# Kernel tuning notes

Measured on AMD Instinct MI355X. Metric: run time of the kernel, lower is better.

Reference implementation:

```python
import jax, jax.numpy as jnp
import numpy as np

K = 2048          # codes per class
NC = 8            # num_classes
CD = 256          # conv_dims
SP = 4            # latent spatial (28 -> 14 -> 7 -> 4)
D = CD * SP * SP  # 4096 codebook vector dim
N = 512           # RoIs


def _conv(x, W, b, stride, pad):
    y = jax.lax.conv_general_dilated(x, W, (stride, stride), [(pad, pad), (pad, pad)],
                                     dimension_numbers=('NCHW', 'OIHW', 'NCHW'))
    return y + b[None, :, None, None]


def _upsample2_ac(x):
    # bilinear upsample x2 with align_corners=True (torch nn.Upsample semantics)
    n, ch, H, W = x.shape
    Ho, Wo = 2 * H, 2 * W
    ys = jnp.arange(Ho) * (H - 1) / (Ho - 1)
    xs = jnp.arange(Wo) * (W - 1) / (Wo - 1)
    y0 = jnp.floor(ys).astype(jnp.int32); y1 = jnp.minimum(y0 + 1, H - 1)
    x0 = jnp.floor(xs).astype(jnp.int32); x1 = jnp.minimum(x0 + 1, W - 1)
    wy = (ys - y0).astype(x.dtype); wx = (xs - x0).astype(x.dtype)
    r = x[:, :, y0, :] * (1 - wy)[None, None, :, None] + x[:, :, y1, :] * wy[None, None, :, None]
    return r[:, :, :, x0] * (1 - wx)[None, None, None, :] + r[:, :, :, x1] * wx[None, None, None, :]


def setup_inputs() -> dict:
    key = jax.random.key(0)
    ks = jax.random.split(key, 20)
    s = 0.02
    inp = {
        'x': jax.random.normal(ks[0], (N, 1, 28, 28), jnp.float32),
        'We0': jax.random.normal(ks[1], (CD, 1, 3, 3), jnp.float32) * s,
        'be0': jnp.zeros((CD,), jnp.float32),
        'We1': jax.random.normal(ks[2], (CD, CD, 3, 3), jnp.float32) * s,
        'be1': jnp.zeros((CD,), jnp.float32),
        'We2': jax.random.normal(ks[3], (CD, CD, 3, 3), jnp.float32) * s,
        'be2': jnp.zeros((CD,), jnp.float32),
        'E': jax.random.normal(ks[4], (K * NC, D), jnp.float32) * s,
        'Wd0': jax.random.normal(ks[5], (CD, CD, 3, 3), jnp.float32) * s,
        'bd0': jnp.zeros((CD,), jnp.float32),
        'Wd1': jax.random.normal(ks[6], (CD, CD, 3, 3), jnp.float32) * s,
        'bd1': jnp.zeros((CD,), jnp.float32),
        'Wd2': jax.random.normal(ks[7], (CD, CD, 3, 3), jnp.float32) * s,
        'bd2': jnp.zeros((CD,), jnp.float32),
        'Wo': jax.random.normal(ks[8], (1, CD, 3, 3), jnp.float32) * s,
        'bo': jnp.zeros((1,), jnp.float32),
        'c': jax.random.randint(ks[9], (N,), 0, NC, jnp.int32),
    }
    return inp


def reference(x, We0, be0, We1, be1, We2, be2, E, Wd0, bd0, Wd1, bd1, Wd2, bd2, Wo, bo, c):
    # ---- encoder: 3 stride-2 convs, relu on all but the last ----
    h = jax.nn.relu(_conv(x, We0, be0, 2, 1))   # [N,CD,14,14]
    h = jax.nn.relu(_conv(h, We1, be1, 2, 1))   # [N,CD,7,7]
    h = _conv(h, We2, be2, 2, 1)                # [N,CD,4,4]
    z_e = h.reshape(N, D)                       # flattened latent, == z_e_x [N,D,1,1]

    # ---- class-conditional VQ ----
    # torch code loops over unique classes and concatenates -> output is in
    # stable-sorted-by-class order; replicate via stable argsort permutation.
    perm = jnp.argsort(c)  # stable
    # distances to the FULL table, then mask codes outside the sample's class slice
    d2 = (jnp.sum(z_e * z_e, axis=1, keepdims=True)         # [N,1]
          - 2.0 * z_e @ E.T                                  # [N,K*NC]
          + jnp.sum(E * E, axis=1)[None, :])
    code_cls = jnp.arange(K * NC, dtype=c.dtype) // K        # class of each code row
    d2 = jnp.where(code_cls[None, :] == c[:, None], d2, jnp.inf)
    idx = jnp.argmin(d2, axis=1)                             # global code index (includes key*K offset)

    q_det = jax.lax.stop_gradient(E)[idx]                    # vq_st uses detached codebook
    z_q_st = z_e + jax.lax.stop_gradient(q_det - z_e)        # straight-through
    z_q_bar = E[idx]                                         # gradient flows to codebook

    z_q_st_p = z_q_st[perm]
    z_q_bar_p = z_q_bar[perm]

    # ---- decoder: (upsample2 bilinear ac + conv + relu) x3, pad=0 on layer k==num_conv-2 ----
    xd = z_q_st_p.reshape(N, CD, SP, SP)
    xd = jax.nn.relu(_conv(_upsample2_ac(xd), Wd0, bd0, 1, 1))  # 4->8
    xd = jax.nn.relu(_conv(_upsample2_ac(xd), Wd1, bd1, 1, 0))  # 8->16->14
    xd = jax.nn.relu(_conv(_upsample2_ac(xd), Wd2, bd2, 1, 1))  # 14->28
    x_tilde = jax.nn.sigmoid(_conv(xd, Wo, bo, 1, 1))           # [N,1,28,28]

    return (x_tilde, z_e.reshape(N, D, 1, 1), z_q_bar_p.reshape(N, D, 1, 1))
```

## Files before the change

### kernel.cpp

```cpp
#include <hip/hip_runtime.h>
#include <hip/hip_bf16.h>
#include <cstdint>
#include <cstddef>

#define CDIV(a,b) (((a)+(b)-1)/(b))

typedef __attribute__((ext_vector_type(8))) short vbf8;
typedef __attribute__((ext_vector_type(4))) float vf4;

__device__ inline unsigned short f2bf(float f) {
  unsigned u = __float_as_uint(f);
  unsigned r = (u + 0x7fffu + ((u >> 16) & 1u)) >> 16;
  return (unsigned short)r;
}
__device__ inline float bf2f(unsigned short h) { return __uint_as_float(((unsigned)h) << 16); }

__global__ __launch_bounds__(256) void conv_e0_cl_kernel(
    const float* __restrict__ x, const float* __restrict__ W,
    const float* __restrict__ b, unsigned short* __restrict__ hi,
    unsigned short* __restrict__ lo)
{
  __shared__ float s_img[784];
  const int n = blockIdx.x;
  const int co = threadIdx.x;
  for (int i = threadIdx.x; i < 784; i += 256) s_img[i] = x[(size_t)n*784 + i];
  float w[9];
#pragma unroll
  for (int t = 0; t < 9; ++t) w[t] = W[co*9 + t];
  const float bb = b[co];
  __syncthreads();
  for (int p = 0; p < 196; ++p) {
    int y = p / 14, xo = p % 14;
    float a = bb;
#pragma unroll
    for (int t = 0; t < 9; ++t) {
      int yi = 2*y + t/3 - 1, xi = 2*xo + t%3 - 1;
      if (yi >= 0 && yi < 28 && xi >= 0 && xi < 28) a = fmaf(w[t], s_img[yi*28 + xi], a);
    }
    a = fmaxf(a, 0.f);
    unsigned short h = f2bf(a);
    size_t oidx = ((size_t)n*196 + p)*256 + co;
    hi[oidx] = h;
    lo[oidx] = f2bf(a - bf2f(h));
  }
}

__global__ __launch_bounds__(256) void wprep2_kernel(
    const float* __restrict__ W, unsigned short* __restrict__ Whi,
    unsigned short* __restrict__ Wlo)
{
  int idx = blockIdx.x*256 + threadIdx.x;
  if (idx >= 589824) return;
  int j   = idx & 7;
  int co  = (idx >> 3) & 255;
  int cig = (idx >> 11) & 31;
  int t   = idx >> 16;
  int ci  = cig*8 + j;
  float w = W[((size_t)co*256 + ci)*9 + t];
  unsigned short h = f2bf(w);
  Whi[idx] = h;
  Wlo[idx] = f2bf(w - bf2f(h));
}

template<int NFM, int WS>
__device__ __forceinline__ void mfma_block(
    const vbf8* __restrict__ sbuf, const vbf8* __restrict__ wsrc, int cc,
    const int (&abase)[NFM], vf4 (&acc)[NFM][4], int cobase, int l15, int lq)
{
#pragma unroll
  for (int t = 0; t < 9; ++t) {
    const int dy = t/3, dx = t%3;
#pragma unroll
    for (int kk = 0; kk < 2; ++kk) {
      vbf8 bfr[4];
      const int cig_g = cc*8 + kk*4 + lq;
#pragma unroll
      for (int nf = 0; nf < 4; ++nf)
        bfr[nf] = wsrc[((size_t)t*32 + cig_g)*256 + cobase + nf*16 + l15];
      vbf8 af[NFM];
      const int cigl = kk*4 + lq;
#pragma unroll
      for (int mf = 0; mf < NFM; ++mf) {
        int lin = abase[mf] + dy*WS + dx;
        af[mf] = sbuf[(lin*8 + cigl) ^ (lin & 7)];
      }
#pragma unroll
      for (int mf = 0; mf < NFM; ++mf)
#pragma unroll
        for (int nf = 0; nf < 4; ++nf)
          acc[mf][nf] = __builtin_amdgcn_mfma_f32_16x16x32_bf16(af[mf], bfr[nf], acc[mf][nf], 0, 0, 0);
    }
  }
}

template<int STRIDE, int HO, int WO, int X0, int WOP, int ROWS, int HI, int WI,
         int PAD, int ACT, int SPLIT, int OUTMODE, int DBUF>
__global__ __launch_bounds__(256, 2) void convmfma_kernel(
    const unsigned short* __restrict__ inT, const unsigned short* __restrict__ inTlo,
    const vbf8* __restrict__ Wt, const vbf8* __restrict__ Wtlo,
    const float* __restrict__ bias,
    unsigned short* __restrict__ outT, unsigned short* __restrict__ outTlo,
    float* __restrict__ outF)
{
  constexpr int NFM = ROWS*WOP/16;
  constexpr int RIN = (ROWS-1)*STRIDE + 3;
  constexpr int WS  = (WOP-1)*STRIDE + 3;
  constexpr int NG  = SPLIT ? 12 : 4;
  constexpr int NELEM = RIN*WS*8;
  constexpr int CEIL = (NELEM + 255) / 256;
  __shared__ vbf8 sA[DBUF ? 2 : 1][NELEM];

  const int n  = blockIdx.x;
  const int y0 = blockIdx.y * ROWS;
  const int tid = threadIdx.x;
  const int lane = tid & 63;
  const int wv = tid >> 6;
  const int l15 = lane & 15;
  const int lq  = lane >> 4;
  const int cobase = wv * 64;

  int abase[NFM];
#pragma unroll
  for (int mf = 0; mf < NFM; ++mf) {
    int pos = mf*16 + l15;
    abase[mf] = (pos / WOP) * STRIDE * WS + (pos % WOP) * STRIDE;
  }

  vf4 acc[NFM][4];
#pragma unroll
  for (int mf = 0; mf < NFM; ++mf)
#pragma unroll
    for (int nf = 0; nf < 4; ++nf) acc[mf][nf] = (vf4){0.f, 0.f, 0.f, 0.f};

  if constexpr (DBUF) {
    int goff[CEIL];
#pragma unroll
    for (int q = 0; q < CEIL; ++q) {
      int idx = tid + q*256;
      int lin = idx >> 3, cig = idx & 7;
      int rr = lin / WS, xx = lin % WS;
      int yi = y0*STRIDE + rr - PAD, xi = X0*STRIDE + xx - PAD;
      bool ok = (idx < NELEM) && yi >= 0 && yi < HI && xi >= 0 && xi < WI;
      goff[q] = ok ? (int)((((size_t)n*HI + yi)*WI + xi)*256 + cig*8) : -1;
    }
    vbf8 r[CEIL];
#pragma unroll
    for (int q = 0; q < CEIL; ++q) {
      vbf8 v = {0,0,0,0,0,0,0,0};
      if (goff[q] >= 0) v = *(const vbf8*)(inT + goff[q]);
      r[q] = v;
    }
#pragma unroll
    for (int q = 0; q < CEIL; ++q) {
      int idx = tid + q*256;
      if (idx < NELEM) { int lin = idx >> 3, cig = idx & 7; sA[0][(lin*8 + cig) ^ (lin & 7)] = r[q]; }
    }
    __syncthreads();
#pragma unroll 1
    for (int g = 0; g < NG; ++g) {
      if (g + 1 < NG) {
        const unsigned short* srcn = (SPLIT && (g+1) >= 8) ? inTlo : inT;
        const int ccn64 = ((g+1) & 3) * 64;
#pragma unroll
        for (int q = 0; q < CEIL; ++q) {
          vbf8 v = {0,0,0,0,0,0,0,0};
          if (goff[q] >= 0) v = *(const vbf8*)(srcn + goff[q] + ccn64);
          r[q] = v;
        }
      }
      const vbf8* wsrc = (SPLIT && g >= 4 && g < 8) ? Wtlo : Wt;
      mfma_block<NFM, WS>(sA[g & 1], wsrc, g & 3, abase, acc, cobase, l15, lq);
      if (g + 1 < NG) {
        vbf8* nb = sA[(g+1) & 1];
#pragma unroll
        for (int q = 0; q < CEIL; ++q) {
          int idx = tid + q*256;
          if (idx < NELEM) { int lin = idx >> 3, cig = idx & 7; nb[(lin*8 + cig) ^ (lin & 7)] = r[q]; }
        }
      }
      __syncthreads();
    }
  } else {
#pragma unroll 1
    for (int g = 0; g < NG; ++g) {
      const int cc = g & 3;
      const unsigned short* src = (SPLIT && g >= 8) ? inTlo : inT;
      const vbf8* wsrc = (SPLIT && g >= 4 && g < 8) ? Wtlo : Wt;
      for (int idx = tid; idx < NELEM; idx += 256) {
        int lin = idx >> 3, cig = idx & 7;
        int rr = lin / WS, xx = lin % WS;
        int yi = y0*STRIDE + rr - PAD, xi = X0*STRIDE + xx - PAD;
        vbf8 v = {0,0,0,0,0,0,0,0};
        if (yi >= 0 && yi < HI && xi >= 0 && xi < WI)
          v = *(const vbf8*)(src + ((((size_t)n*HI + yi)*WI + xi)*256 + cc*64 + cig*8));
        sA[0][(lin*8 + cig) ^ (lin & 7)] = v;
      }
      __syncthreads();
      mfma_block<NFM, WS>(sA[0], wsrc, cc, abase, acc, cobase, l15, lq);
      __syncthreads();
    }
  }

  float bb[4];
#pragma unroll
  for (int nf = 0; nf < 4; ++nf) bb[nf] = bias[cobase + nf*16 + l15];
#pragma unroll
  for (int mf = 0; mf < NFM; ++mf) {
#pragma unroll
    for (int q = 0; q < 4; ++q) {
      int pos = mf*16 + lq*4 + q;
      int y = y0 + pos/WOP, x = X0 + pos % WOP;
      if (X0 + WOP > WO && x >= WO) continue;
      if (HO % ROWS != 0 && y >= HO) continue;
#pragma unroll
      for (int nf = 0; nf < 4; ++nf) {
        float v = acc[mf][nf][q] + bb[nf];
        if (ACT) v = fmaxf(v, 0.f);
        const int co = cobase + nf*16 + l15;
        if (OUTMODE == 2) {
          outF[((size_t)n*256 + co)*(HO*WO) + y*WO + x] = v;
        } else {
          size_t oidx = (((size_t)n*HO + y)*WO + x)*256 + co;
          unsigned short h = f2bf(v);
          outT[oidx] = h;
          if (OUTMODE == 1) outTlo[oidx] = f2bf(v - bf2f(h));
        }
      }
    }
  }
}

template<int H, int W>
__global__ __launch_bounds__(256) void upsample_cl_kernel(
    const unsigned short* __restrict__ in, unsigned short* __restrict__ out, int nimg)
{
  constexpr int Ho = 2*H, Wo = 2*W;
  int idx = blockIdx.x*256 + threadIdx.x;
  int total = nimg * Ho * Wo * 32;
  if (idx >= total) return;
  int cig = idx & 31; int rest = idx >> 5;
  int xo = rest % Wo; rest /= Wo;
  int yo = rest % Ho; int n = rest / Ho;
  float ys = (float)(yo*(H-1)) / (float)(Ho-1);
  float xs = (float)(xo*(W-1)) / (float)(Wo-1);
  int ya = (int)ys; int yb = (ya+1 < H) ? ya+1 : H-1;
  int xa = (int)xs; int xb = (xa+1 < W) ? xa+1 : W-1;
  float wy = ys - (float)ya, wx = xs - (float)xa;
  const unsigned short* base = in + (size_t)n*H*W*256 + cig*8;
  vbf8 vaa = *(const vbf8*)(base + ((size_t)ya*W + xa)*256);
  vbf8 vab = *(const vbf8*)(base + ((size_t)ya*W + xb)*256);
  vbf8 vba = *(const vbf8*)(base + ((size_t)yb*W + xa)*256);
  vbf8 vbb = *(const vbf8*)(base + ((size_t)yb*W + xb)*256);
  vbf8 o;
#pragma unroll
  for (int j = 0; j < 8; ++j) {
    float r0 = bf2f((unsigned short)vaa[j])*(1.f-wy) + bf2f((unsigned short)vba[j])*wy;
    float r1 = bf2f((unsigned short)vab[j])*(1.f-wy) + bf2f((unsigned short)vbb[j])*wy;
    o[j] = (short)f2bf(r0*(1.f-wx) + r1*wx);
  }
  *(vbf8*)(out + (((size_t)n*Ho + yo)*Wo + xo)*256 + cig*8) = o;
}

__global__ __launch_bounds__(256) void conv_out_t_kernel(
    const unsigned short* __restrict__ a2t, const float* __restrict__ Wo,
    const float* __restrict__ bo, float* __restrict__ out)
{
  const int n = blockIdx.x;
  const int y0 = blockIdx.y * 14;
  const int tid = threadIdx.x;
  __shared__ vbf8 s_in[16*30*8];
  __shared__ float s_w[9*64];
  float acc[2] = {0.f, 0.f};
  for (int cc = 0; cc < 4; ++cc) {
    for (int idx = tid; idx < 16*30*8; idx += 256) {
      int lin = idx >> 3, cig = idx & 7;
      int r = lin / 30, xx = lin % 30;
      int yi = y0 + r - 1, xi = xx - 1;
      vbf8 v = {0,0,0,0,0,0,0,0};
      if (yi >= 0 && yi < 28 && xi >= 0 && xi < 28)
        v = *(const vbf8*)(a2t + (((size_t)n*28 + yi)*28 + xi)*256 + cc*64 + cig*8);
      s_in[(lin*8 + cig) ^ (lin & 7)] = v;
    }
    for (int idx = tid; idx < 576; idx += 256) {
      int t = idx / 64, cil = idx % 64;
      s_w[t*64 + cil] = Wo[((size_t)cc*64 + cil)*9 + t];
    }
    __syncthreads();
#pragma unroll
    for (int q = 0; q < 2; ++q) {
      int p = tid + q*256;
      if (p < 392) {
        int y = p / 28, x = p % 28;
        float a = acc[q];
#pragma unroll
        for (int t = 0; t < 9; ++t) {
          int lin = (y + t/3)*30 + (x + t%3);
#pragma unroll
          for (int cig = 0; cig < 8; ++cig) {
            vbf8 v = s_in[(lin*8 + cig) ^ (lin & 7)];
#pragma unroll
            for (int j = 0; j < 8; ++j)
              a = fmaf(bf2f((unsigned short)v[j]), s_w[t*64 + cig*8 + j], a);
          }
        }
        acc[q] = a;
      }
    }
    __syncthreads();
  }
  const float bb = bo[0];
  for (int q = 0; q < 2; ++q) {
    int p = tid + q*256;
    if (p < 392) {
      int y = y0 + p/28, x = p%28;
      out[(size_t)n*784 + y*28 + x] = 1.f/(1.f + expf(-(acc[q] + bb)));
    }
  }
}

__global__ __launch_bounds__(256) void enorm_kernel(
    const float* __restrict__ E, float* __restrict__ norms)
{
  const int k = blockIdx.x;
  const float4* row = (const float4*)(E + (size_t)k*4096);
  float s = 0.f;
  for (int i = threadIdx.x; i < 1024; i += 256) {
    float4 v = row[i];
    s += v.x*v.x + v.y*v.y + v.z*v.z + v.w*v.w;
  }
  __shared__ float red[256];
  red[threadIdx.x] = s; __syncthreads();
  for (int off = 128; off > 0; off >>= 1) {
    if (threadIdx.x < off) red[threadIdx.x] += red[threadIdx.x + off];
    __syncthreads();
  }
  if (threadIdx.x == 0) norms[k] = red[0];
}

__global__ __launch_bounds__(256) void etrans_kernel(
    const float* __restrict__ E, unsigned short* __restrict__ Et)
{
  const int cb = blockIdx.x;
  const int kb = blockIdx.y;
  const int t = threadIdx.x;
  const int cl = t >> 2;
  const int seg = t & 3;
  const int code = cb*64 + cl;
  const int k0 = kb*64 + seg*16;
  const float4* src = (const float4*)(E + (size_t)code*4096 + k0);
  float4 v0 = src[0], v1 = src[1], v2 = src[2], v3 = src[3];
  vbf8 a, b;
  a[0]=(short)f2bf(v0.x); a[1]=(short)f2bf(v0.y); a[2]=(short)f2bf(v0.z); a[3]=(short)f2bf(v0.w);
  a[4]=(short)f2bf(v1.x); a[5]=(short)f2bf(v1.y); a[6]=(short)f2bf(v1.z); a[7]=(short)f2bf(v1.w);
  b[0]=(short)f2bf(v2.x); b[1]=(short)f2bf(v2.y); b[2]=(short)f2bf(v2.z); b[3]=(short)f2bf(v2.w);
  b[4]=(short)f2bf(v3.x); b[5]=(short)f2bf(v3.y); b[6]=(short)f2bf(v3.z); b[7]=(short)f2bf(v3.w);
  vbf8* dst = (vbf8*)Et;
  dst[(size_t)(k0 >> 3)*16384 + code]     = a;
  dst[((size_t)(k0 >> 3) + 1)*16384 + code] = b;
}

__global__ __launch_bounds__(512) void perm_kernel(
    const int* __restrict__ c, int* __restrict__ perm, int* __restrict__ off)
{
  __shared__ int sc[512];
  __shared__ int cnt[8];
  __shared__ int base[9];
  const int i = threadIdx.x;
  sc[i] = c[i];
  if (i < 8) cnt[i] = 0;
  __syncthreads();
  atomicAdd(&cnt[sc[i]], 1);
  __syncthreads();
  if (i == 0) { int a = 0; for (int j = 0; j < 8; ++j) { base[j] = a; a += cnt[j]; } base[8] = a; }
  __syncthreads();
  const int ci = sc[i];
  int rank = 0;
  for (int j = 0; j < i; ++j) rank += (sc[j] == ci) ? 1 : 0;
  perm[base[ci] + rank] = i;
  if (i < 9) off[i] = base[i];
}

__global__ __launch_bounds__(256) void vq_coarse_kernel(
    const float* __restrict__ zE, const vbf8* __restrict__ Etv,
    const float* __restrict__ norms, const int* __restrict__ perm,
    const int* __restrict__ offs, float* __restrict__ dco)
{
  const int cls = blockIdx.x;
  const int mb  = blockIdx.y;
  const int kb  = blockIdx.z;
  const int s0 = offs[cls];
  const int total = offs[cls+1] - s0;
  int nrows = total - mb*64;
  if (nrows <= 0) return;
  if (nrows > 64) nrows = 64;

  __shared__ vbf8 sA[64*8];
  __shared__ int srow_s[64];
  const int tid = threadIdx.x;
  if (tid < 64) srow_s[tid] = (tid < nrows) ? perm[s0 + mb*64 + tid] : -1;
  __syncthreads();

  const int lane = tid & 63;
  const int wv = tid >> 6;
  const int l15 = lane & 15;
  const int lq  = lane >> 4;

  const int myrow = tid >> 2;
  const int seg = tid & 3;
  const int srow_mine = srow_s[myrow];
  const float* zbase = (srow_mine >= 0) ? (zE + (size_t)srow_mine*4096 + seg*16) : nullptr;

  const int cbase = cls*2048 + kb*256 + wv*64;

  vf4 acc[4][4];
#pragma unroll
  for (int mf = 0; mf < 4; ++mf)
#pragma unroll
    for (int nf = 0; nf < 4; ++nf) acc[mf][nf] = (vf4){0.f, 0.f, 0.f, 0.f};

#pragma unroll 1
  for (int k0 = 0; k0 < 4096; k0 += 64) {
    {
      float4 v0, v1, v2, v3;
      if (zbase) {
        const float4* p = (const float4*)(zbase + k0);
        v0 = p[0]; v1 = p[1]; v2 = p[2]; v3 = p[3];
      } else {
        v0 = v1 = v2 = v3 = (float4){0.f, 0.f, 0.f, 0.f};
      }
      vbf8 a, b;
      a[0]=(short)f2bf(v0.x); a[1]=(short)f2bf(v0.y); a[2]=(short)f2bf(v0.z); a[3]=(short)f2bf(v0.w);
      a[4]=(short)f2bf(v1.x); a[5]=(short)f2bf(v1.y); a[6]=(short)f2bf(v1.z); a[7]=(short)f2bf(v1.w);
      b[0]=(short)f2bf(v2.x); b[1]=(short)f2bf(v2.y); b[2]=(short)f2bf(v2.z); b[3]=(short)f2bf(v2.w);
      b[4]=(short)f2bf(v3.x); b[5]=(short)f2bf(v3.y); b[6]=(short)f2bf(v3.z); b[7]=(short)f2bf(v3.w);
      int c0 = seg*2;
      sA[myrow*8 + (c0 ^ (myrow & 7))]       = a;
      sA[myrow*8 + ((c0 + 1) ^ (myrow & 7))] = b;
    }
    __syncthreads();
#pragma unroll
    for (int kb32 = 0; kb32 < 2; ++kb32) {
      vbf8 af[4], bf[4];
#pragma unroll
      for (int mf = 0; mf < 4; ++mf) {
        int row = mf*16 + l15;
        af[mf] = sA[row*8 + ((kb32*4 + lq) ^ (row & 7))];
      }
      const size_t kg = (size_t)((k0 >> 3) + kb32*4 + lq);
#pragma unroll
      for (int nf = 0; nf < 4; ++nf)
        bf[nf] = Etv[kg*16384 + cbase + nf*16 + l15];
#pragma unroll
      for (int mf = 0; mf < 4; ++mf)
#pragma unroll
        for (int nf = 0; nf < 4; ++nf)
          acc[mf][nf] = __builtin_amdgcn_mfma_f32_16x16x32_bf16(af[mf], bf[nf], acc[mf][nf], 0, 0, 0);
    }
    __syncthreads();
  }

  float nrm[4];
#pragma unroll
  for (int nf = 0; nf < 4; ++nf) nrm[nf] = norms[cbase + nf*16 + l15];
#pragma unroll
  for (int mf = 0; mf < 4; ++mf) {
#pragma unroll
    for (int q = 0; q < 4; ++q) {
      int slot = mf*16 + lq*4 + q;
      if (slot < nrows) {
        int s = srow_s[slot];
        float* drow = dco + (size_t)s*2048 + (kb*256 + wv*64);
#pragma unroll
        for (int nf = 0; nf < 4; ++nf)
          drow[nf*16 + l15] = nrm[nf] - 2.f*acc[mf][nf][q];
      }
    }
  }
}

__global__ __launch_bounds__(256) void vq_select_kernel(
    const float* __restrict__ dco, const int* __restrict__ c,
    const float* __restrict__ zE, const float* __restrict__ E,
    int* __restrict__ codes)
{
  const int s = blockIdx.x;
  const int cls = c[s];
  const int tid = threadIdx.x;
  const float* drow = dco + (size_t)s*2048;

  float mn = 3.4e38f, mx = -3.4e38f;
  for (int j = tid; j < 2048; j += 256) {
    float d = drow[j];
    mn = fminf(mn, d); mx = fmaxf(mx, d);
  }
  __shared__ float smn[256], smx[256];
  smn[tid] = mn; smx[tid] = mx;
  __syncthreads();
  for (int o = 128; o > 0; o >>= 1) {
    if (tid < o) { smn[tid] = fminf(smn[tid], smn[tid+o]); smx[tid] = fmaxf(smx[tid], smx[tid+o]); }
    __syncthreads();
  }
  const float dmin = smn[0], dmax = smx[0];
  const float margin = 0.06f*(dmax - dmin) + 1e-6f*fabsf(dmin) + 1e-20f;

  __shared__ int cand[64];
  __shared__ int cnt_s;
  if (tid == 0) cnt_s = 0;
  __syncthreads();
  for (int j = tid; j < 2048; j += 256) {
    if (drow[j] <= dmin + margin) {
      int p = atomicAdd(&cnt_s, 1);
      if (p < 64) cand[p] = j;
    }
  }
  __syncthreads();
  const int cnt = (cnt_s < 64) ? cnt_s : 64;

  __shared__ double red[256];
  __shared__ double bestd_s;
  __shared__ int bestc_s;
  if (tid == 0) { bestd_s = 1.0e300; bestc_s = 0x7fffffff; }
  __syncthreads();
  const float* zrow = zE + (size_t)s*4096;
  for (int t = 0; t < cnt; ++t) {
    const int gcode = cls*2048 + cand[t];
    const float* erow = E + (size_t)gcode*4096;
    double p = 0.0;
    for (int e2 = tid; e2 < 4096; e2 += 256) {
      double ev = (double)erow[e2];
      double zv = (double)zrow[e2];
      p += ev*ev - 2.0*zv*ev;
    }
    red[tid] = p;
    __syncthreads();
    for (int o = 128; o > 0; o >>= 1) {
      if (tid < o) red[tid] += red[tid+o];
      __syncthreads();
    }
    if (tid == 0) {
      double d = red[0];
      if (d < bestd_s || (d == bestd_s && gcode < bestc_s)) { bestd_s = d; bestc_s = gcode; }
    }
    __syncthreads();
  }
  if (tid == 0) codes[s] = bestc_s;
}

__global__ __launch_bounds__(256) void gather_t_kernel(
    const int* __restrict__ codes, const int* __restrict__ perm,
    const float* __restrict__ E, float* __restrict__ zq, unsigned short* __restrict__ zqt)
{
  const int i = blockIdx.x;
  const int s = perm[i];
  const int code = codes[s];
  const float4* src = (const float4*)(E + (size_t)code*4096);
  float4* dst = (float4*)(zq + (size_t)i*4096);
  for (int t = threadIdx.x; t < 1024; t += 256) {
    float4 v = src[t];
    dst[t] = v;
    int e0 = t*4;
    int ci = e0 >> 4, sp = e0 & 15;
    unsigned short* zp = zqt + ((size_t)i*16 + sp)*256 + ci;
    zp[0]   = f2bf(v.x);
    zp[256] = f2bf(v.y);
    zp[512] = f2bf(v.z);
    zp[768] = f2bf(v.w);
  }
}

extern "C" void kernel_launch(void* const* d_in, const int* in_sizes, int n_in,
                              void* d_out, int out_size, void* d_ws, size_t ws_size,
                              hipStream_t stream) {
  const float* x   = (const float*)d_in[0];
  const float* We0 = (const float*)d_in[1];
  const float* be0 = (const float*)d_in[2];
  const float* We1 = (const float*)d_in[3];
  const float* be1 = (const float*)d_in[4];
  const float* We2 = (const float*)d_in[5];
  const float* be2 = (const float*)d_in[6];
  const float* E   = (const float*)d_in[7];
  const float* Wd0 = (const float*)d_in[8];
  const float* bd0 = (const float*)d_in[9];
  const float* Wd1 = (const float*)d_in[10];
  const float* bd1 = (const float*)d_in[11];
  const float* Wd2 = (const float*)d_in[12];
  const float* bd2 = (const float*)d_in[13];
  const float* Wo  = (const float*)d_in[14];
  const float* bo  = (const float*)d_in[15];
  const int*   c   = (const int*)d_in[16];

  float* out = (float*)d_out;
  float* z_e = out + (size_t)512*784;
  float* zq  = z_e + (size_t)512*4096;

  char* ws = (char*)d_ws;
  size_t off = 0;
  float* norms = (float*)(ws + off); off += 65536;
  int* codes = (int*)(ws + off); off += 2048;
  int* perm = (int*)(ws + off); off += 2048;
  int* offs = (int*)(ws + off); off += 256;
  float* dco = (float*)(ws + off); off += (size_t)512*2048*4;
  unsigned short* zqt = (unsigned short*)(ws + off); off += (size_t)512*16*256*2;
  unsigned short* Et = (unsigned short*)(ws + off); off += (size_t)512*16384*8*2;
  unsigned short* Wt0  = (unsigned short*)(ws + off); off += 1179648;
  unsigned short* Wt0l = (unsigned short*)(ws + off); off += 1179648;
  unsigned short* Wt1  = (unsigned short*)(ws + off); off += 1179648;
  unsigned short* Wt1l = (unsigned short*)(ws + off); off += 1179648;
  unsigned short* Wt2  = (unsigned short*)(ws + off); off += 1179648;
  unsigned short* Wt2l = (unsigned short*)(ws + off); off += 1179648;
  unsigned short* We1h = (unsigned short*)(ws + off); off += 1179648;
  unsigned short* We1l = (unsigned short*)(ws + off); off += 1179648;
  unsigned short* We2h = (unsigned short*)(ws + off); off += 1179648;
  unsigned short* We2l = (unsigned short*)(ws + off); off += 1179648;
  char* big = ws + off;
  size_t avail = (ws_size > off) ? ws_size - off : 0;

  int NB = 512;
  while (NB > 1 && (size_t)NB * 1350656ull > avail) NB >>= 1;
  const int nch = 512 / NB;

  size_t o = 0;
  unsigned short* h0h = (unsigned short*)(big + o); o += (size_t)NB*100352;
  unsigned short* h0l = (unsigned short*)(big + o); o += (size_t)NB*100352;
  unsigned short* h1h = (unsigned short*)(big + o); o += (size_t)NB*25088;
  unsigned short* h1l = (unsigned short*)(big + o); o += (size_t)NB*25088;
  unsigned short* u0t = (unsigned short*)(big + o); o += (size_t)NB*32768;
  unsigned short* a0t = (unsigned short*)(big + o); o += (size_t)NB*32768;
  unsigned short* u1t = (unsigned short*)(big + o); o += (size_t)NB*131072;
  unsigned short* a1t = (unsigned short*)(big + o); o += (size_t)NB*100352;
  unsigned short* u2t = (unsigned short*)(big + o); o += (size_t)NB*401408;
  unsigned short* a2t = (unsigned short*)(big + o); o += (size_t)NB*401408;

  wprep2_kernel<<<CDIV(589824,256), 256, 0, stream>>>(Wd0, Wt0, Wt0l);
  wprep2_kernel<<<CDIV(589824,256), 256, 0, stream>>>(Wd1, Wt1, Wt1l);
  wprep2_kernel<<<CDIV(589824,256), 256, 0, stream>>>(Wd2, Wt2, Wt2l);
  wprep2_kernel<<<CDIV(589824,256), 256, 0, stream>>>(We1, We1h, We1l);
  wprep2_kernel<<<CDIV(589824,256), 256, 0, stream>>>(We2, We2h, We2l);
  enorm_kernel<<<16384, 256, 0, stream>>>(E, norms);
  etrans_kernel<<<dim3(256,64), 256, 0, stream>>>(E, Et);

  for (int ch = 0; ch < nch; ++ch) {
    conv_e0_cl_kernel<<<NB, 256, 0, stream>>>(x + (size_t)ch*NB*784, We0, be0, h0h, h0l);
    convmfma_kernel<2,7,7,0,8,4, 14,14,1,1,1,1, 1><<<dim3(NB,2), 256, 0, stream>>>(
        h0h, h0l, (const vbf8*)We1h, (const vbf8*)We1l, be1, h1h, h1l, nullptr);
    convmfma_kernel<2,4,4,0,4,4, 7,7,1,0,1,2, 1><<<dim3(NB,1), 256, 0, stream>>>(
        h1h, h1l, (const vbf8*)We2h, (const vbf8*)We2l, be2, nullptr, nullptr,
        z_e + (size_t)ch*NB*4096);
  }
  perm_kernel<<<1, 512, 0, stream>>>(c, perm, offs);
  vq_coarse_kernel<<<dim3(8,8,8), 256, 0, stream>>>(
      z_e, (const vbf8*)Et, norms, perm, offs, dco);
  vq_select_kernel<<<512, 256, 0, stream>>>(dco, c, z_e, E, codes);
  gather_t_kernel<<<512, 256, 0, stream>>>(codes, perm, E, zq, zqt);

  for (int ch = 0; ch < nch; ++ch) {
    const unsigned short* zt = zqt + (size_t)ch*NB*16*256;
    upsample_cl_kernel<4,4><<<CDIV(NB*2048,256), 256, 0, stream>>>(zt, u0t, NB);
    convmfma_kernel<1,8,8,0,8,8, 8,8,1,1,0,0, 1><<<dim3(NB,1), 256, 0, stream>>>(
        u0t, nullptr, (const vbf8*)Wt0, nullptr, bd0, a0t, nullptr, nullptr);
    upsample_cl_kernel<8,8><<<CDIV(NB*8192,256), 256, 0, stream>>>(a0t, u1t, NB);
    convmfma_kernel<1,14,14,0,16,4, 16,16,0,1,0,0, 1><<<dim3(NB,4), 256, 0, stream>>>(
        u1t, nullptr, (const vbf8*)Wt1, nullptr, bd1, a1t, nullptr, nullptr);
    upsample_cl_kernel<14,14><<<CDIV(NB*25088,256), 256, 0, stream>>>(a1t, u2t, NB);
    convmfma_kernel<1,28,28,0,28,4, 28,28,1,1,0,0, 0><<<dim3(NB,7), 256, 0, stream>>>(
        u2t, nullptr, (const vbf8*)Wt2, nullptr, bd2, a2t, nullptr, nullptr);
    conv_out_t_kernel<<<dim3(NB,2), 256, 0, stream>>>(a2t, Wo, bo, out + (size_t)ch*NB*784);
  }
}
```

Measured before the change: 1.812 ms.

## Widen conv input-channel chunk per stage and fuse codebook norm with transpose

Convolution kernels gain a CIG template parameter, so most layers stage 128 input channels per LDS chunk instead of 64. This halves the number of load/sync stages and makes each MFMA block longer. The cost is a larger LDS footprint, which may lower occupancy and change bank-conflict behaviour under the XOR swizzle. Separately, the codebook norm and bf16 transpose kernels are merged into one pass, so E is read once instead of twice.

```diff
diff --git a/kernel.cpp b/kernel.cpp
--- a/kernel.cpp
+++ b/kernel.cpp
@@ -62,18 +62,19 @@
   Wlo[idx] = f2bf(w - bf2f(h));
 }
 
-template<int NFM, int WS>
+template<int NFM, int WS, int CIG>
 __device__ __forceinline__ void mfma_block(
     const vbf8* __restrict__ sbuf, const vbf8* __restrict__ wsrc, int cc,
     const int (&abase)[NFM], vf4 (&acc)[NFM][4], int cobase, int l15, int lq)
 {
+  constexpr int NKK = CIG/4;
 #pragma unroll
   for (int t = 0; t < 9; ++t) {
     const int dy = t/3, dx = t%3;
 #pragma unroll
-    for (int kk = 0; kk < 2; ++kk) {
+    for (int kk = 0; kk < NKK; ++kk) {
       vbf8 bfr[4];
-      const int cig_g = cc*8 + kk*4 + lq;
+      const int cig_g = cc*CIG + kk*4 + lq;
 #pragma unroll
       for (int nf = 0; nf < 4; ++nf)
         bfr[nf] = wsrc[((size_t)t*32 + cig_g)*256 + cobase + nf*16 + l15];
@@ -82,7 +83,7 @@
 #pragma unroll
       for (int mf = 0; mf < NFM; ++mf) {
         int lin = abase[mf] + dy*WS + dx;
-        af[mf] = sbuf[(lin*8 + cigl) ^ (lin & 7)];
+        af[mf] = sbuf[(lin*CIG + cigl) ^ (lin & 7)];
       }
 #pragma unroll
       for (int mf = 0; mf < NFM; ++mf)
@@ -94,7 +95,7 @@
 }
 
 template<int STRIDE, int HO, int WO, int X0, int WOP, int ROWS, int HI, int WI,
-         int PAD, int ACT, int SPLIT, int OUTMODE, int DBUF>
+         int PAD, int ACT, int SPLIT, int OUTMODE, int DBUF, int CIG>
 __global__ __launch_bounds__(256, 2) void convmfma_kernel(
     const unsigned short* __restrict__ inT, const unsigned short* __restrict__ inTlo,
     const vbf8* __restrict__ Wt, const vbf8* __restrict__ Wtlo,
@@ -105,8 +106,9 @@
   constexpr int NFM = ROWS*WOP/16;
   constexpr int RIN = (ROWS-1)*STRIDE + 3;
   constexpr int WS  = (WOP-1)*STRIDE + 3;
-  constexpr int NG  = SPLIT ? 12 : 4;
-  constexpr int NELEM = RIN*WS*8;
+  constexpr int NCC = 256/(CIG*8);
+  constexpr int NG  = SPLIT ? 3*NCC : NCC;
+  constexpr int NELEM = RIN*WS*CIG;
   constexpr int CEIL = (NELEM + 255) / 256;
   __shared__ vbf8 sA[DBUF ? 2 : 1][NELEM];
 
@@ -137,7 +139,7 @@
 #pragma unroll
     for (int q = 0; q < CEIL; ++q) {
       int idx = tid + q*256;
-      int lin = idx >> 3, cig = idx & 7;
+      int lin = idx / CIG, cig = idx % CIG;
       int rr = lin / WS, xx = lin % WS;
       int yi = y0*STRIDE + rr - PAD, xi = X0*STRIDE + xx - PAD;
       bool ok = (idx < NELEM) && yi >= 0 && yi < HI && xi >= 0 && xi < WI;
@@ -153,29 +155,31 @@
 #pragma unroll
     for (int q = 0; q < CEIL; ++q) {
       int idx = tid + q*256;
-      if (idx < NELEM) { int lin = idx >> 3, cig = idx & 7; sA[0][(lin*8 + cig) ^ (lin & 7)] = r[q]; }
+      if (idx < NELEM) { int lin = idx / CIG, cig = idx % CIG; sA[0][(lin*CIG + cig) ^ (lin & 7)] = r[q]; }
     }
     __syncthreads();
 #pragma unroll 1
     for (int g = 0; g < NG; ++g) {
       if (g + 1 < NG) {
-        const unsigned short* srcn = (SPLIT && (g+1) >= 8) ? inTlo : inT;
-        const int ccn64 = ((g+1) & 3) * 64;
+        const int passn = (g+1) / NCC;
+        const unsigned short* srcn = (SPLIT && passn == 2) ? inTlo : inT;
+        const int ccn = ((g+1) % NCC) * (CIG*8);
 #pragma unroll
         for (int q = 0; q < CEIL; ++q) {
           vbf8 v = {0,0,0,0,0,0,0,0};
-          if (goff[q] >= 0) v = *(const vbf8*)(srcn + goff[q] + ccn64);
+          if (goff[q] >= 0) v = *(const vbf8*)(srcn + goff[q] + ccn);
           r[q] = v;
         }
       }
-      const vbf8* wsrc = (SPLIT && g >= 4 && g < 8) ? Wtlo : Wt;
-      mfma_block<NFM, WS>(sA[g & 1], wsrc, g & 3, abase, acc, cobase, l15, lq);
+      const int pass = g / NCC;
+      const vbf8* wsrc = (SPLIT && pass == 1) ? Wtlo : Wt;
+      mfma_block<NFM, WS, CIG>(sA[g & 1], wsrc, g % NCC, abase, acc, cobase, l15, lq);
       if (g + 1 < NG) {
         vbf8* nb = sA[(g+1) & 1];
 #pragma unroll
         for (int q = 0; q < CEIL; ++q) {
           int idx = tid + q*256;
-          if (idx < NELEM) { int lin = idx >> 3, cig = idx & 7; nb[(lin*8 + cig) ^ (lin & 7)] = r[q]; }
+          if (idx < NELEM) { int lin = idx / CIG, cig = idx % CIG; nb[(lin*CIG + cig) ^ (lin & 7)] = r[q]; }
         }
       }
       __syncthreads();
@@ -183,20 +187,21 @@
   } else {
 #pragma unroll 1
     for (int g = 0; g < NG; ++g) {
-      const int cc = g & 3;
-      const unsigned short* src = (SPLIT && g >= 8) ? inTlo : inT;
-      const vbf8* wsrc = (SPLIT && g >= 4 && g < 8) ? Wtlo : Wt;
+      const int pass = g / NCC;
+      const int cc = g % NCC;
+      const unsigned short* src = (SPLIT && pass == 2) ? inTlo : inT;
+      const vbf8* wsrc = (SPLIT && pass == 1) ? Wtlo : Wt;
       for (int idx = tid; idx < NELEM; idx += 256) {
-        int lin = idx >> 3, cig = idx & 7;
+        int lin = idx / CIG, cig = idx % CIG;
         int rr = lin / WS, xx = lin % WS;
         int yi = y0*STRIDE + rr - PAD, xi = X0*STRIDE + xx - PAD;
         vbf8 v = {0,0,0,0,0,0,0,0};
         if (yi >= 0 && yi < HI && xi >= 0 && xi < WI)
-          v = *(const vbf8*)(src + ((((size_t)n*HI + yi)*WI + xi)*256 + cc*64 + cig*8));
-        sA[0][(lin*8 + cig) ^ (lin & 7)] = v;
+          v = *(const vbf8*)(src + ((((size_t)n*HI + yi)*WI + xi)*256 + cc*(CIG*8) + cig*8));
+        sA[0][(lin*CIG + cig) ^ (lin & 7)] = v;
       }
       __syncthreads();
-      mfma_block<NFM, WS>(sA[0], wsrc, cc, abase, acc, cobase, l15, lq);
+      mfma_block<NFM, WS, CIG>(sA[0], wsrc, cc, abase, acc, cobase, l15, lq);
       __syncthreads();
     }
   }
@@ -318,45 +323,32 @@
   }
 }
 
-__global__ __launch_bounds__(256) void enorm_kernel(
-    const float* __restrict__ E, float* __restrict__ norms)
-{
-  const int k = blockIdx.x;
-  const float4* row = (const float4*)(E + (size_t)k*4096);
-  float s = 0.f;
-  for (int i = threadIdx.x; i < 1024; i += 256) {
-    float4 v = row[i];
-    s += v.x*v.x + v.y*v.y + v.z*v.z + v.w*v.w;
-  }
-  __shared__ float red[256];
-  red[threadIdx.x] = s; __syncthreads();
-  for (int off = 128; off > 0; off >>= 1) {
-    if (threadIdx.x < off) red[threadIdx.x] += red[threadIdx.x + off];
-    __syncthreads();
-  }
-  if (threadIdx.x == 0) norms[k] = red[0];
-}
-
-__global__ __launch_bounds__(256) void etrans_kernel(
-    const float* __restrict__ E, unsigned short* __restrict__ Et)
+__global__ __launch_bounds__(256) void eprep_kernel(
+    const float* __restrict__ E, unsigned short* __restrict__ Et,
+    float* __restrict__ norms)
 {
   const int cb = blockIdx.x;
-  const int kb = blockIdx.y;
-  const int t = threadIdx.x;
-  const int cl = t >> 2;
-  const int seg = t & 3;
+  const int tid = threadIdx.x;
+  const int cl = tid >> 2;
+  const int seg = tid & 3;
   const int code = cb*64 + cl;
-  const int k0 = kb*64 + seg*16;
-  const float4* src = (const float4*)(E + (size_t)code*4096 + k0);
-  float4 v0 = src[0], v1 = src[1], v2 = src[2], v3 = src[3];
-  vbf8 a, b;
-  a[0]=(short)f2bf(v0.x); a[1]=(short)f2bf(v0.y); a[2]=(short)f2bf(v0.z); a[3]=(short)f2bf(v0.w);
-  a[4]=(short)f2bf(v1.x); a[5]=(short)f2bf(v1.y); a[6]=(short)f2bf(v1.z); a[7]=(short)f2bf(v1.w);
-  b[0]=(short)f2bf(v2.x); b[1]=(short)f2bf(v2.y); b[2]=(short)f2bf(v2.z); b[3]=(short)f2bf(v2.w);
-  b[4]=(short)f2bf(v3.x); b[5]=(short)f2bf(v3.y); b[6]=(short)f2bf(v3.z); b[7]=(short)f2bf(v3.w);
+  const float4* srcRow = (const float4*)(E + (size_t)code*4096);
   vbf8* dst = (vbf8*)Et;
-  dst[(size_t)(k0 >> 3)*16384 + code]     = a;
-  dst[((size_t)(k0 >> 3) + 1)*16384 + code] = b;
+  float nacc = 0.f;
+#pragma unroll 4
+  for (int g8 = 0; g8 < 128; ++g8) {
+    const int kg = g8*4 + seg;
+    float4 a = srcRow[kg*2], b = srcRow[kg*2 + 1];
+    nacc += a.x*a.x + a.y*a.y + a.z*a.z + a.w*a.w
+          + b.x*b.x + b.y*b.y + b.z*b.z + b.w*b.w;
+    vbf8 v;
+    v[0]=(short)f2bf(a.x); v[1]=(short)f2bf(a.y); v[2]=(short)f2bf(a.z); v[3]=(short)f2bf(a.w);
+    v[4]=(short)f2bf(b.x); v[5]=(short)f2bf(b.y); v[6]=(short)f2bf(b.z); v[7]=(short)f2bf(b.w);
+    dst[(size_t)kg*16384 + code] = v;
+  }
+  nacc += __shfl_xor(nacc, 1);
+  nacc += __shfl_xor(nacc, 2);
+  if (seg == 0) norms[code] = nacc;
 }
 
 __global__ __launch_bounds__(512) void perm_kernel(
@@ -636,14 +628,13 @@
   wprep2_kernel<<<CDIV(589824,256), 256, 0, stream>>>(Wd2, Wt2, Wt2l);
   wprep2_kernel<<<CDIV(589824,256), 256, 0, stream>>>(We1, We1h, We1l);
   wprep2_kernel<<<CDIV(589824,256), 256, 0, stream>>>(We2, We2h, We2l);
-  enorm_kernel<<<16384, 256, 0, stream>>>(E, norms);
-  etrans_kernel<<<dim3(256,64), 256, 0, stream>>>(E, Et);
+  eprep_kernel<<<256, 256, 0, stream>>>(E, Et, norms);
 
   for (int ch = 0; ch < nch; ++ch) {
     conv_e0_cl_kernel<<<NB, 256, 0, stream>>>(x + (size_t)ch*NB*784, We0, be0, h0h, h0l);
-    convmfma_kernel<2,7,7,0,8,4, 14,14,1,1,1,1, 1><<<dim3(NB,2), 256, 0, stream>>>(
+    convmfma_kernel<2,7,7,0,8,4, 14,14,1,1,1,1, 1,8><<<dim3(NB,2), 256, 0, stream>>>(
         h0h, h0l, (const vbf8*)We1h, (const vbf8*)We1l, be1, h1h, h1l, nullptr);
-    convmfma_kernel<2,4,4,0,4,4, 7,7,1,0,1,2, 1><<<dim3(NB,1), 256, 0, stream>>>(
+    convmfma_kernel<2,4,4,0,4,4, 7,7,1,0,1,2, 1,16><<<dim3(NB,1), 256, 0, stream>>>(
         h1h, h1l, (const vbf8*)We2h, (const vbf8*)We2l, be2, nullptr, nullptr,
         z_e + (size_t)ch*NB*4096);
   }
@@ -656,13 +647,13 @@
   for (int ch = 0; ch < nch; ++ch) {
     const unsigned short* zt = zqt + (size_t)ch*NB*16*256;
     upsample_cl_kernel<4,4><<<CDIV(NB*2048,256), 256, 0, stream>>>(zt, u0t, NB);
-    convmfma_kernel<1,8,8,0,8,8, 8,8,1,1,0,0, 1><<<dim3(NB,1), 256, 0, stream>>>(
+    convmfma_kernel<1,8,8,0,8,8, 8,8,1,1,0,0, 1,16><<<dim3(NB,1), 256, 0, stream>>>(
         u0t, nullptr, (const vbf8*)Wt0, nullptr, bd0, a0t, nullptr, nullptr);
     upsample_cl_kernel<8,8><<<CDIV(NB*8192,256), 256, 0, stream>>>(a0t, u1t, NB);
-    convmfma_kernel<1,14,14,0,16,4, 16,16,0,1,0,0, 1><<<dim3(NB,4), 256, 0, stream>>>(
+    convmfma_kernel<1,14,14,0,16,4, 16,16,0,1,0,0, 1,16><<<dim3(NB,4), 256, 0, stream>>>(
         u1t, nullptr, (const vbf8*)Wt1, nullptr, bd1, a1t, nullptr, nullptr);
     upsample_cl_kernel<14,14><<<CDIV(NB*25088,256), 256, 0, stream>>>(a1t, u2t, NB);
-    convmfma_kernel<1,28,28,0,28,4, 28,28,1,1,0,0, 0><<<dim3(NB,7), 256, 0, stream>>>(
+    convmfma_kernel<1,28,28,0,28,4, 28,28,1,1,0,0, 0,16><<<dim3(NB,7), 256, 0, stream>>>(
         u2t, nullptr, (const vbf8*)Wt2, nullptr, bd2, a2t, nullptr, nullptr);
     conv_out_t_kernel<<<dim3(NB,2), 256, 0, stream>>>(a2t, Wo, bo, out + (size_t)ch*NB*784);
   }
```

New measurement: 2.404 ms. 32.7% more time.
